# Optimization experiments

Measured on AMD Instinct MI355X. Metric: run time of the kernel, lower is better.

Reference implementation:

```python
import jax, jax.numpy as jnp
import numpy as np

EPS = 1e-5
NEG_INF = float('-inf')

B, L, D = 4, 1024, 1024
H = 16
HD = D // H
I = 3280  # _round_to_multiple(3.2 * 1024, 8)
WIN = 256
STD = 0.01


def rmsnorm(x, w):
    x = jnp.clip(x.astype(jnp.float32), -10000.0, 10000.0)
    rms = jnp.sqrt(jnp.maximum(jnp.mean(x * x, axis=-1, keepdims=True), EPS) + EPS)
    out = x / rms * w
    return jnp.where(jnp.isfinite(out), out, jnp.zeros_like(out))


def setup_inputs() -> dict:
    key = jax.random.key(0)
    ks = jax.random.split(key, 12)
    inp = {
        'x': jax.random.normal(ks[0], (B, L, D), dtype=jnp.float32),
        'wq_w': jax.random.normal(ks[1], (D, D), dtype=jnp.float32) * STD,
        'wq_b': jnp.zeros((D,), jnp.float32),
        'wk_w': jax.random.normal(ks[2], (D, D), dtype=jnp.float32) * STD,
        'wk_b': jnp.zeros((D,), jnp.float32),
        'wv_w': jax.random.normal(ks[3], (D, D), dtype=jnp.float32) * STD,
        'wv_b': jnp.zeros((D,), jnp.float32),
        'wo_w': jax.random.normal(ks[4], (D, D), dtype=jnp.float32) * STD,
        'wo_b': jnp.zeros((D,), jnp.float32),
        'q_norm_w': jnp.ones((HD,), jnp.float32),
        'k_norm_w': jnp.ones((HD,), jnp.float32),
        'seq_norm_w': jnp.ones((D,), jnp.float32),
        'seq_post_norm_w': jnp.ones((D,), jnp.float32),
        'ffn_norm_w': jnp.ones((D,), jnp.float32),
        'ffn_post_norm_w': jnp.ones((D,), jnp.float32),
        'w1_w': jax.random.normal(ks[5], (I, D), dtype=jnp.float32) * STD,
        'w1_b': jnp.zeros((I,), jnp.float32),
        'w2_w': jax.random.normal(ks[6], (D, I), dtype=jnp.float32) * STD,
        'w2_b': jnp.zeros((D,), jnp.float32),
        'w3_w': jax.random.normal(ks[7], (I, D), dtype=jnp.float32) * STD,
        'w3_b': jnp.zeros((I,), jnp.float32),
        'window_size': WIN,
    }
    return inp


def attention(x, wq_w, wq_b, wk_w, wk_b, wv_w, wv_b, wo_w, wo_b, q_norm_w, k_norm_w, window_size):
    b, l, d = x.shape
    x = x.astype(jnp.float32)
    q = (x @ wq_w.T + wq_b).reshape(b, l, H, HD)
    k = (x @ wk_w.T + wk_b).reshape(b, l, H, HD)
    v = (x @ wv_w.T + wv_b).reshape(b, l, H, HD)
    q = rmsnorm(q, q_norm_w)
    k = rmsnorm(k, k_norm_w)
    scale = HD ** -0.5
    scores = jnp.einsum('blhd,bmhd->bhlm', q, k) * scale
    i = jnp.arange(l)[:, None]
    j = jnp.arange(l)[None, :]
    masked = (j > i) | (i - j >= window_size)  # True => forbidden
    scores = scores + jnp.where(masked, NEG_INF, 0.0)
    p = jax.nn.softmax(scores, axis=-1)
    attn = jnp.einsum('bhlm,bmhd->blhd', p, v)
    attn = jnp.where(jnp.isfinite(attn), attn, jnp.zeros_like(attn))
    attn = attn.reshape(b, l, d)
    return attn @ wo_w.T + wo_b


def swiglu(x, w1_w, w1_b, w2_w, w2_b, w3_w, w3_b):
    x = x.astype(jnp.float32)
    z1 = x @ w1_w.T + w1_b
    z3 = x @ w3_w.T + w3_b
    return (jax.nn.silu(z1) * z3) @ w2_w.T + w2_b


def reference(x, wq_w, wq_b, wk_w, wk_b, wv_w, wv_b, wo_w, wo_b,
              q_norm_w, k_norm_w, seq_norm_w, seq_post_norm_w,
              ffn_norm_w, ffn_post_norm_w,
              w1_w, w1_b, w2_w, w2_b, w3_w, w3_b, window_size):
    # seq_norm -> attn -> seq_post_norm -> residual
    a = attention(rmsnorm(x, seq_norm_w), wq_w, wq_b, wk_w, wk_b, wv_w, wv_b,
                  wo_w, wo_b, q_norm_w, k_norm_w, window_size)
    h = x + rmsnorm(a, seq_post_norm_w)
    # ffn_norm -> ffn -> ffn_post_norm -> residual
    f = swiglu(rmsnorm(h, ffn_norm_w), w1_w, w1_b, w2_w, w2_b, w3_w, w3_b)
    return h + rmsnorm(f, ffn_post_norm_w)
```

## Files before the change

### kernel.cpp

```cpp
#include <hip/hip_runtime.h>
#include <cmath>
#include <cstdint>

typedef __bf16 bf16;
typedef bf16 bf16x4 __attribute__((ext_vector_type(4)));
typedef bf16 bf16x8 __attribute__((ext_vector_type(8)));
typedef float f32x4 __attribute__((ext_vector_type(4)));
typedef unsigned int u32;
typedef u32 u32x4 __attribute__((ext_vector_type(4)));

#define EPS 1e-5f

__device__ __forceinline__ float clipf(float v) {
    return fminf(fmaxf(v, -10000.0f), 10000.0f);
}
__device__ __forceinline__ float fin0(float v) { return isfinite(v) ? v : 0.0f; }

__device__ __forceinline__ void async_copy16(void* lds, const void* g) {
    __builtin_amdgcn_global_load_lds((__attribute__((address_space(1))) void*)(void*)g,
                                     (__attribute__((address_space(3))) void*)lds,
                                     16, 0, 0);
}

__global__ __launch_bounds__(256) void prep(const float* __restrict__ wq, const float* __restrict__ wk,
                                            const float* __restrict__ wv, const float* __restrict__ wo,
                                            bf16* __restrict__ Wq, bf16* __restrict__ Wk,
                                            bf16* __restrict__ Wv, bf16* __restrict__ Wo,
                                            const float* __restrict__ w1, const float* __restrict__ w3,
                                            bf16* __restrict__ Wf,
                                            const float* __restrict__ w2, bf16* __restrict__ W2p,
                                            const float* __restrict__ x, const float* __restrict__ snw,
                                            bf16* __restrict__ xn) {
    const int bid = blockIdx.x, t = threadIdx.x;
    if (bid < 4096) {
        int z = bid >> 10, r = bid & 1023;
        const float* in = (z == 0) ? wq : (z == 1) ? wk : (z == 2) ? wv : wo;
        bf16* out = (z == 0) ? Wq : (z == 1) ? Wk : (z == 2) ? Wv : Wo;
        f32x4 v = ((const f32x4*)(in + (size_t)r * 1024))[t];
        bf16x4 o = {(bf16)v[0], (bf16)v[1], (bf16)v[2], (bf16)v[3]};
        ((bf16x4*)(out + (size_t)r * 1024))[t] = o;
    } else if (bid < 10752) {
        int ri = bid - 4096;
        int lc = ((ri >> 5) << 4) + (ri & 15);
        const float* in = ((ri >> 4) & 1) ? w3 : w1;
        bf16x4 o = {(bf16)0.f, (bf16)0.f, (bf16)0.f, (bf16)0.f};
        if (lc < 3280) {
            f32x4 v = ((const f32x4*)(in + (size_t)lc * 1024))[t];
            o[0] = (bf16)v[0]; o[1] = (bf16)v[1]; o[2] = (bf16)v[2]; o[3] = (bf16)v[3];
        }
        ((bf16x4*)(Wf + (size_t)ri * 1024))[t] = o;
    } else if (bid < 11776) {
        int r = bid - 10752;
        for (int c4 = t * 4; c4 < 3328; c4 += 1024) {
            bf16x4 o = {(bf16)0.f, (bf16)0.f, (bf16)0.f, (bf16)0.f};
            if (c4 + 3 < 3280) {
                f32x4 v = *(const f32x4*)(w2 + (size_t)r * 3280 + c4);
                o[0] = (bf16)v[0]; o[1] = (bf16)v[1]; o[2] = (bf16)v[2]; o[3] = (bf16)v[3];
            } else {
                #pragma unroll
                for (int j = 0; j < 4; ++j)
                    if (c4 + j < 3280) o[j] = (bf16)w2[(size_t)r * 3280 + c4 + j];
            }
            *(bf16x4*)(W2p + (size_t)r * 3328 + c4) = o;
        }
    } else {
        __shared__ float sred[4];
        int row = bid - 11776;
        f32x4 xv = ((const f32x4*)(x + (size_t)row * 1024))[t];
        f32x4 cv;
        cv[0] = clipf(xv[0]); cv[1] = clipf(xv[1]); cv[2] = clipf(xv[2]); cv[3] = clipf(xv[3]);
        float ss = cv[0]*cv[0] + cv[1]*cv[1] + cv[2]*cv[2] + cv[3]*cv[3];
        #pragma unroll
        for (int off = 32; off >= 1; off >>= 1) ss += __shfl_xor(ss, off, 64);
        if ((t & 63) == 0) sred[t >> 6] = ss;
        __syncthreads();
        float tot = sred[0] + sred[1] + sred[2] + sred[3];
        float rms = sqrtf(fmaxf(tot * (1.0f / 1024.0f), EPS) + EPS);
        f32x4 wv_ = ((const f32x4*)snw)[t];
        bf16x4 o;
        o[0] = (bf16)fin0(cv[0] / rms * wv_[0]);
        o[1] = (bf16)fin0(cv[1] / rms * wv_[1]);
        o[2] = (bf16)fin0(cv[2] / rms * wv_[2]);
        o[3] = (bf16)fin0(cv[3] / rms * wv_[3]);
        *(bf16x4*)(xn + (size_t)row * 1024 + t * 4) = o;
    }
}

__global__ __launch_bounds__(256) void gemm_qkv(const bf16* __restrict__ A,
                                                const bf16* __restrict__ B0,
                                                const bf16* __restrict__ B1,
                                                const bf16* __restrict__ B2,
                                                const float* __restrict__ g0,
                                                const float* __restrict__ g1,
                                                const float* __restrict__ g2,
                                                const float* __restrict__ qnw,
                                                const float* __restrict__ knw,
                                                bf16* __restrict__ C0,
                                                bf16* __restrict__ C1,
                                                bf16* __restrict__ VT) {
    const int z = blockIdx.z;
    const bf16* B = (z == 0) ? B0 : (z == 1) ? B1 : B2;
    const float* bias = (z == 0) ? g0 : (z == 1) ? g1 : g2;
    const float* hw = (z == 0) ? qnw : knw;

    __shared__ __align__(16) bf16 sA[2][128 * 32];
    __shared__ __align__(16) bf16 sB[2][128 * 32];
    const int tid = threadIdx.x;
    const int w = tid >> 6, lane = tid & 63;
    const int m0 = blockIdx.x * 128;
    const int n0 = blockIdx.y * 128;
    const int mwo = (w >> 1) * 64, nwo = (w & 1) * 64;
    const int r16 = lane & 15, quad = lane >> 4;
    const int kreg = quad * 8;
    const int K = 1024, N = 1024;

    f32x4 zero = {0.f, 0.f, 0.f, 0.f};
    f32x4 acc[4][4];
    #pragma unroll
    for (int i = 0; i < 4; ++i)
        #pragma unroll
        for (int j = 0; j < 4; ++j) acc[i][j] = zero;

    const int c0 = tid, c1 = tid + 256;
    const int am0 = c0 >> 2, ak0 = (c0 & 3) << 3;
    const int am1 = c1 >> 2, ak1 = (c1 & 3) << 3;

    {
        async_copy16(&sA[0][c0 * 8], &A[(size_t)(m0 + am0) * K + ak0]);
        async_copy16(&sA[0][c1 * 8], &A[(size_t)(m0 + am1) * K + ak1]);
        async_copy16(&sB[0][c0 * 8], &B[(size_t)(n0 + am0) * K + ak0]);
        async_copy16(&sB[0][c1 * 8], &B[(size_t)(n0 + am1) * K + ak1]);
    }
    for (int kt = 0; kt < 32; ++kt) {
        __syncthreads();
        const int cur = kt & 1, nxt = cur ^ 1;
        if (kt + 1 < 32) {
            const int kb = (kt + 1) << 5;
            async_copy16(&sA[nxt][c0 * 8], &A[(size_t)(m0 + am0) * K + kb + ak0]);
            async_copy16(&sA[nxt][c1 * 8], &A[(size_t)(m0 + am1) * K + kb + ak1]);
            async_copy16(&sB[nxt][c0 * 8], &B[(size_t)(n0 + am0) * K + kb + ak0]);
            async_copy16(&sB[nxt][c1 * 8], &B[(size_t)(n0 + am1) * K + kb + ak1]);
        }
        bf16x8 af[4], bfr[4];
        #pragma unroll
        for (int i = 0; i < 4; ++i) {
            af[i]  = *(const bf16x8*)&sA[cur][(mwo + i * 16 + r16) * 32 + kreg];
            bfr[i] = *(const bf16x8*)&sB[cur][(nwo + i * 16 + r16) * 32 + kreg];
        }
        #pragma unroll
        for (int mi = 0; mi < 4; ++mi)
            #pragma unroll
            for (int ni = 0; ni < 4; ++ni)
                acc[mi][ni] = __builtin_amdgcn_mfma_f32_16x16x32_bf16(af[mi], bfr[ni], acc[mi][ni], 0, 0, 0);
    }

    float bv[4];
    #pragma unroll
    for (int ni = 0; ni < 4; ++ni) bv[ni] = bias[n0 + nwo + ni * 16 + r16];

    if (z < 2) {
        bf16* C = (z == 0) ? C0 : C1;
        float nwv[4];
        #pragma unroll
        for (int ni = 0; ni < 4; ++ni) nwv[ni] = hw[ni * 16 + r16];
        #pragma unroll
        for (int mi = 0; mi < 4; ++mi) {
            #pragma unroll
            for (int r = 0; r < 4; ++r) {
                float v[4], ss = 0.0f;
                #pragma unroll
                for (int ni = 0; ni < 4; ++ni) {
                    v[ni] = clipf(acc[mi][ni][r] + bv[ni]);
                    ss += v[ni] * v[ni];
                }
                ss += __shfl_xor(ss, 1, 64);
                ss += __shfl_xor(ss, 2, 64);
                ss += __shfl_xor(ss, 4, 64);
                ss += __shfl_xor(ss, 8, 64);
                float rms = sqrtf(fmaxf(ss * (1.0f / 64.0f), EPS) + EPS);
                int row = m0 + mwo + mi * 16 + quad * 4 + r;
                #pragma unroll
                for (int ni = 0; ni < 4; ++ni) {
                    int col = n0 + nwo + ni * 16 + r16;
                    C[(size_t)row * N + col] = (bf16)fin0(v[ni] / rms * nwv[ni]);
                }
            }
        }
    } else {
        const int b_ = m0 >> 10;
        const int tokbase = (m0 & 1023) + mwo;
        #pragma unroll
        for (int ni = 0; ni < 4; ++ni) {
            int col = n0 + nwo + ni * 16 + r16;
            int h_ = col >> 6, hd = col & 63;
            bf16* dst = VT + (((size_t)b_ * 16 + h_) * 64 + hd) * 1024;
            #pragma unroll
            for (int mi = 0; mi < 4; ++mi) {
                bf16x4 pack;
                #pragma unroll
                for (int r = 0; r < 4; ++r) pack[r] = (bf16)(acc[mi][ni][r] + bv[ni]);
                *(bf16x4*)&dst[tokbase + mi * 16 + quad * 4] = pack;
            }
        }
    }
}

__global__ __launch_bounds__(256) void attn_win(const bf16* __restrict__ q,
                                                const bf16* __restrict__ k,
                                                const bf16* __restrict__ vt,
                                                const int* __restrict__ winp,
                                                bf16* __restrict__ o) {
    __shared__ __align__(16) bf16 sQ[64 * 64];
    __shared__ __align__(16) bf16 sK[64 * 64];
    __shared__ __align__(16) bf16 sVt[64 * 80];
    __shared__ __align__(16) bf16 sP[64 * 64];
    const int tid = threadIdx.x, w = tid >> 6, lane = tid & 63;
    const int qt = blockIdx.x, h = blockIdx.y, b = blockIdx.z;
    const int q0 = qt * 64;
    const int win = *winp;
    const float scale = 0.125f;
    const int r16 = lane & 15, quad = lane >> 4;

    {
        int qr0 = tid >> 3, col0 = (tid & 7) * 8;
        async_copy16(&sQ[tid * 8], &q[(((size_t)b * 1024 + q0 + qr0) * 16 + h) * 64 + col0]);
        int c1 = tid + 256;
        int qr1 = c1 >> 3, col1 = (c1 & 7) * 8;
        async_copy16(&sQ[c1 * 8], &q[(((size_t)b * 1024 + q0 + qr1) * 16 + h) * 64 + col1]);
    }
    __syncthreads();
    bf16x8 aq0 = *(const bf16x8*)&sQ[(w * 16 + r16) * 64 + quad * 8];
    bf16x8 aq1 = *(const bf16x8*)&sQ[(w * 16 + r16) * 64 + 32 + quad * 8];

    float Lr[4];
    f32x4 zero = {0.f, 0.f, 0.f, 0.f};
    f32x4 accO[4];
    #pragma unroll
    for (int r = 0; r < 4; ++r) Lr[r] = 0.0f;
    #pragma unroll
    for (int nf = 0; nf < 4; ++nf) accO[nf] = zero;

    int lo = q0 - (win - 1); if (lo < 0) lo = 0;
    const int kt0 = lo >> 6;
    const bf16* vth = vt + ((size_t)b * 16 + h) * 64 * 1024;

    for (int kt = kt0; kt <= qt; ++kt) {
        __syncthreads();
        {
            int col0 = (tid & 7) * 8;
            async_copy16(&sK[tid * 8], &k[(((size_t)b * 1024 + kt * 64 + (tid >> 3)) * 16 + h) * 64 + col0]);
            int c1 = tid + 256;
            int col1 = (c1 & 7) * 8;
            async_copy16(&sK[c1 * 8], &k[(((size_t)b * 1024 + kt * 64 + (c1 >> 3)) * 16 + h) * 64 + col1]);
        }
        #pragma unroll
        for (int c = tid; c < 512; c += 256) {
            int hd = c >> 3, koff = (c & 7) * 8;
            *(u32x4*)&sVt[hd * 80 + koff] = *(const u32x4*)&vth[(size_t)hd * 1024 + kt * 64 + koff];
        }
        __syncthreads();

        f32x4 sf[4];
        #pragma unroll
        for (int nf = 0; nf < 4; ++nf) {
            bf16x8 bk0 = *(const bf16x8*)&sK[(nf * 16 + r16) * 64 + quad * 8];
            bf16x8 bk1 = *(const bf16x8*)&sK[(nf * 16 + r16) * 64 + 32 + quad * 8];
            f32x4 accS = zero;
            accS = __builtin_amdgcn_mfma_f32_16x16x32_bf16(aq0, bk0, accS, 0, 0, 0);
            accS = __builtin_amdgcn_mfma_f32_16x16x32_bf16(aq1, bk1, accS, 0, 0, 0);
            sf[nf] = accS;
        }

        #pragma unroll
        for (int r = 0; r < 4; ++r) {
            int i = q0 + w * 16 + quad * 4 + r;
            float ps = 0.0f;
            #pragma unroll
            for (int nf = 0; nf < 4; ++nf) {
                int j = kt * 64 + nf * 16 + r16;
                bool ok = (j <= i) && (i - j < win);
                float pv = ok ? __expf(sf[nf][r] * scale - 8.0f) : 0.0f;
                ps += pv;
                sP[(w * 16 + quad * 4 + r) * 64 + nf * 16 + r16] = (bf16)pv;
            }
            Lr[r] += ps;
        }
        __syncthreads();

        bf16x8 ap0 = *(const bf16x8*)&sP[(w * 16 + r16) * 64 + quad * 8];
        bf16x8 ap1 = *(const bf16x8*)&sP[(w * 16 + r16) * 64 + 32 + quad * 8];
        #pragma unroll
        for (int nf = 0; nf < 4; ++nf) {
            bf16x8 bv0 = *(const bf16x8*)&sVt[(nf * 16 + r16) * 80 + quad * 8];
            bf16x8 bv1 = *(const bf16x8*)&sVt[(nf * 16 + r16) * 80 + 32 + quad * 8];
            accO[nf] = __builtin_amdgcn_mfma_f32_16x16x32_bf16(ap0, bv0, accO[nf], 0, 0, 0);
            accO[nf] = __builtin_amdgcn_mfma_f32_16x16x32_bf16(ap1, bv1, accO[nf], 0, 0, 0);
        }
    }

    #pragma unroll
    for (int r = 0; r < 4; ++r) {
        float l = Lr[r];
        l += __shfl_xor(l, 1, 64);
        l += __shfl_xor(l, 2, 64);
        l += __shfl_xor(l, 4, 64);
        l += __shfl_xor(l, 8, 64);
        float inv = (l > 0.0f) ? 1.0f / l : 0.0f;
        int row = q0 + w * 16 + quad * 4 + r;
        #pragma unroll
        for (int nf = 0; nf < 4; ++nf) {
            float ov = fin0(accO[nf][r] * inv);
            o[(((size_t)b * 1024 + row) * 16 + h) * 64 + nf * 16 + r16] = (bf16)ov;
        }
    }
}

__global__ __launch_bounds__(512) void gemm_sk2(const bf16* __restrict__ A,
                                                const bf16* __restrict__ B,
                                                float* __restrict__ P,
                                                int K, int Kh) {
    __shared__ __align__(16) bf16 sA[2][256 * 32];
    __shared__ __align__(16) bf16 sB[2][128 * 32];
    const int tid = threadIdx.x;
    const int w = tid >> 6, lane = tid & 63;
    const int m0 = blockIdx.x * 256, n0 = blockIdx.y * 128;
    const int mwo = (w & 3) * 64, nwo = (w >> 2) * 64;
    const int r16 = lane & 15, quad = lane >> 4, kreg = quad * 8;
    const int kbase = blockIdx.z * Kh;
    const int N = 1024;

    const int ar0 = tid >> 2,        ak0 = (tid & 3) << 3;
    const int c1 = tid + 512;
    const int ar1 = c1 >> 2,         ak1 = (c1 & 3) << 3;
    const int br = tid >> 2,         bk = (tid & 3) << 3;

    f32x4 zero = {0.f, 0.f, 0.f, 0.f};
    f32x4 acc[4][4];
    #pragma unroll
    for (int i = 0; i < 4; ++i)
        #pragma unroll
        for (int j = 0; j < 4; ++j) acc[i][j] = zero;

    {
        async_copy16(&sA[0][tid * 8], &A[(size_t)(m0 + ar0) * K + kbase + ak0]);
        async_copy16(&sA[0][c1 * 8],  &A[(size_t)(m0 + ar1) * K + kbase + ak1]);
        async_copy16(&sB[0][tid * 8], &B[(size_t)(n0 + br) * K + kbase + bk]);
    }
    const int kIters = Kh >> 5;
    for (int kt = 0; kt < kIters; ++kt) {
        __syncthreads();
        const int cur = kt & 1, nxt = cur ^ 1;
        if (kt + 1 < kIters) {
            const int kb = kbase + ((kt + 1) << 5);
            async_copy16(&sA[nxt][tid * 8], &A[(size_t)(m0 + ar0) * K + kb + ak0]);
            async_copy16(&sA[nxt][c1 * 8],  &A[(size_t)(m0 + ar1) * K + kb + ak1]);
            async_copy16(&sB[nxt][tid * 8], &B[(size_t)(n0 + br) * K + kb + bk]);
        }
        bf16x8 af[4], bfr[4];
        #pragma unroll
        for (int i = 0; i < 4; ++i) {
            af[i]  = *(const bf16x8*)&sA[cur][(mwo + i * 16 + r16) * 32 + kreg];
            bfr[i] = *(const bf16x8*)&sB[cur][(nwo + i * 16 + r16) * 32 + kreg];
        }
        #pragma unroll
        for (int mi = 0; mi < 4; ++mi)
            #pragma unroll
            for (int ni = 0; ni < 4; ++ni)
                acc[mi][ni] = __builtin_amdgcn_mfma_f32_16x16x32_bf16(af[mi], bfr[ni], acc[mi][ni], 0, 0, 0);
    }

    float* Pz = P + (size_t)blockIdx.z * 4096 * 1024;
    #pragma unroll
    for (int mi = 0; mi < 4; ++mi)
        #pragma unroll
        for (int ni = 0; ni < 4; ++ni) {
            int col = n0 + nwo + ni * 16 + r16;
            #pragma unroll
            for (int r = 0; r < 4; ++r) {
                int row = m0 + mwo + mi * 16 + quad * 4 + r;
                Pz[(size_t)row * N + col] = acc[mi][ni][r];
            }
        }
}

template <bool EMIT>
__global__ __launch_bounds__(512) void resid_norm(const float* __restrict__ xres,
                                                  const float* __restrict__ p0,
                                                  const float* __restrict__ p1,
                                                  const float* __restrict__ bias,
                                                  const float* __restrict__ wpost,
                                                  const float* __restrict__ wnext,
                                                  float* __restrict__ hout,
                                                  bf16* __restrict__ hnout) {
    __shared__ float sred[8];
    const int tid = threadIdx.x;
    const int grp = tid >> 8, t = tid & 255;
    const int w4 = (tid >> 6) & 3;
    for (int it = 0; it < 4; ++it) {
        int row = it * 1024 + blockIdx.x * 2 + grp;
        f32x4 a0 = ((const f32x4*)(p0 + (size_t)row * 1024))[t];
        f32x4 a1 = ((const f32x4*)(p1 + (size_t)row * 1024))[t];
        f32x4 bv = ((const f32x4*)bias)[t];
        f32x4 af;
        af[0] = clipf(a0[0] + a1[0] + bv[0]);
        af[1] = clipf(a0[1] + a1[1] + bv[1]);
        af[2] = clipf(a0[2] + a1[2] + bv[2]);
        af[3] = clipf(a0[3] + a1[3] + bv[3]);
        float ss = af[0]*af[0] + af[1]*af[1] + af[2]*af[2] + af[3]*af[3];
        #pragma unroll
        for (int off = 32; off >= 1; off >>= 1) ss += __shfl_xor(ss, off, 64);
        __syncthreads();
        if ((tid & 63) == 0) sred[grp * 4 + w4] = ss;
        __syncthreads();
        float tot = sred[grp*4+0] + sred[grp*4+1] + sred[grp*4+2] + sred[grp*4+3];
        float rms1 = sqrtf(fmaxf(tot * (1.0f / 1024.0f), EPS) + EPS);
        f32x4 xv = ((const f32x4*)(xres + (size_t)row * 1024))[t];
        f32x4 wp = ((const f32x4*)wpost)[t];
        f32x4 hv;
        hv[0] = xv[0] + fin0(af[0] / rms1 * wp[0]);
        hv[1] = xv[1] + fin0(af[1] / rms1 * wp[1]);
        hv[2] = xv[2] + fin0(af[2] / rms1 * wp[2]);
        hv[3] = xv[3] + fin0(af[3] / rms1 * wp[3]);
        ((f32x4*)(hout + (size_t)row * 1024))[t] = hv;
        if (EMIT) {
            f32x4 cv;
            cv[0] = clipf(hv[0]); cv[1] = clipf(hv[1]); cv[2] = clipf(hv[2]); cv[3] = clipf(hv[3]);
            float ss2 = cv[0]*cv[0] + cv[1]*cv[1] + cv[2]*cv[2] + cv[3]*cv[3];
            #pragma unroll
            for (int off = 32; off >= 1; off >>= 1) ss2 += __shfl_xor(ss2, off, 64);
            __syncthreads();
            if ((tid & 63) == 0) sred[grp * 4 + w4] = ss2;
            __syncthreads();
            float tot2 = sred[grp*4+0] + sred[grp*4+1] + sred[grp*4+2] + sred[grp*4+3];
            float rms2 = sqrtf(fmaxf(tot2 * (1.0f / 1024.0f), EPS) + EPS);
            f32x4 wn = ((const f32x4*)wnext)[t];
            bf16x4 o;
            o[0] = (bf16)fin0(cv[0] / rms2 * wn[0]);
            o[1] = (bf16)fin0(cv[1] / rms2 * wn[1]);
            o[2] = (bf16)fin0(cv[2] / rms2 * wn[2]);
            o[3] = (bf16)fin0(cv[3] / rms2 * wn[3]);
            *(bf16x4*)(hnout + (size_t)row * 1024 + t * 4) = o;
        }
    }
}

template <int MB>
__device__ __forceinline__ void mquad(const bf16x8 (&a)[2][2], const bf16x8 (&breg)[4][2],
                                      f32x4 (&acc)[8][4]) {
    __builtin_amdgcn_s_setprio(1);
    #pragma unroll
    for (int n = 0; n < 4; ++n) {
        acc[MB][n]     = __builtin_amdgcn_mfma_f32_16x16x32_bf16(a[0][0], breg[n][0], acc[MB][n], 0, 0, 0);
        acc[MB][n]     = __builtin_amdgcn_mfma_f32_16x16x32_bf16(a[0][1], breg[n][1], acc[MB][n], 0, 0, 0);
        acc[MB + 1][n] = __builtin_amdgcn_mfma_f32_16x16x32_bf16(a[1][0], breg[n][0], acc[MB + 1][n], 0, 0, 0);
        acc[MB + 1][n] = __builtin_amdgcn_mfma_f32_16x16x32_bf16(a[1][1], breg[n][1], acc[MB + 1][n], 0, 0, 0);
    }
    __builtin_amdgcn_s_setprio(0);
}

__device__ __forceinline__ void aread(const bf16* Ah, int MB, int r16, int koff0, int koff1,
                                      bf16x8 (&a)[2][2]) {
    const bf16* p0 = &Ah[(MB * 16 + r16) * 64];
    const bf16* p1 = &Ah[((MB + 1) * 16 + r16) * 64];
    a[0][0] = *(const bf16x8*)&p0[koff0];
    a[0][1] = *(const bf16x8*)&p0[koff1];
    a[1][0] = *(const bf16x8*)&p1[koff0];
    a[1][1] = *(const bf16x8*)&p1[koff1];
}

__global__ __launch_bounds__(512, 2) void gemm_ffn1_8ph(const bf16* __restrict__ A,
                                                        const bf16* __restrict__ Wf,
                                                        const float* __restrict__ b1,
                                                        const float* __restrict__ b3,
                                                        bf16* __restrict__ G) {
    __shared__ __align__(16) bf16 sA[2][2][128 * 64];
    __shared__ __align__(16) bf16 sB[2][2][128 * 64];
    const int tid = threadIdx.x;
    const int w = tid >> 6, lane = tid & 63;
    const int wr = w >> 2, wc = w & 3;
    const int r16 = lane & 15, quad = lane >> 4;

    const int flat = blockIdx.x;
    const int swb = (flat & 7) * 52 + (flat >> 3);
    const int bm = swb & 15, bn = swb >> 4;
    const int m0 = bm * 256;
    const int n0i = bn * 256;

    const int swz = r16 & 7;
    const int koff0 = ((quad ^ swz) << 3);
    const int koff1 = (((quad + 4) ^ swz) << 3);

    const int sr0 = tid >> 3, sr1 = sr0 + 64;
    const int sk0 = (((tid & 7) ^ (sr0 & 7)) << 3);

    const bf16* aSrc0 = A + (size_t)m0 * 1024;
    const bf16* aSrc1 = A + (size_t)(m0 + 128) * 1024;
    const bf16* bSrc0 = Wf + (size_t)n0i * 1024;
    const bf16* bSrc1 = Wf + (size_t)(n0i + 128) * 1024;

#define STAGE(dst, src, ktile) do {                                                        \
        async_copy16(&(dst)[tid * 8],         (src) + (size_t)sr0 * 1024 + (ktile) * 64 + sk0); \
        async_copy16(&(dst)[(tid + 512) * 8], (src) + (size_t)sr1 * 1024 + (ktile) * 64 + sk0); \
    } while (0)

    f32x4 acc[8][4];
    #pragma unroll
    for (int i = 0; i < 8; ++i)
        #pragma unroll
        for (int j = 0; j < 4; ++j) acc[i][j] = (f32x4){0.f, 0.f, 0.f, 0.f};

    STAGE(sA[0][0], aSrc0, 0); STAGE(sA[0][1], aSrc1, 0);
    STAGE(sB[0][0], bSrc0, 0); STAGE(sB[0][1], bSrc1, 0);
    STAGE(sB[1][0], bSrc0, 1); STAGE(sB[1][1], bSrc1, 1);
    asm volatile("s_waitcnt vmcnt(4)" ::: "memory");
    __builtin_amdgcn_sched_barrier(0);

    for (int t = 0; t < 16; ++t) {
        const int cur = t & 1, nxt = cur ^ 1;
        const bf16* Ah = &sA[cur][wr][0];
        const bf16* Bh = &sB[cur][wc >> 1][0];
        const int rbB = (wc & 1) << 6;

        __builtin_amdgcn_s_barrier();
        if (t + 1 < 16) { STAGE(sA[nxt][0], aSrc0, t + 1); STAGE(sA[nxt][1], aSrc1, t + 1); }

        bf16x8 breg[4][2];
        #pragma unroll
        for (int n = 0; n < 4; ++n) {
            const bf16* p = &Bh[(rbB + n * 16 + r16) * 64];
            breg[n][0] = *(const bf16x8*)&p[koff0];
            breg[n][1] = *(const bf16x8*)&p[koff1];
        }
        bf16x8 a0[2][2], a1[2][2];
        aread(Ah, 0, r16, koff0, koff1, a0);
        aread(Ah, 2, r16, koff0, koff1, a1);
        mquad<0>(a0, breg, acc);

        asm volatile("s_waitcnt lgkmcnt(0)" ::: "memory");
        __builtin_amdgcn_sched_barrier(0);
        __builtin_amdgcn_s_barrier();
        if (t + 2 < 16) { STAGE(sB[cur][0], bSrc0, t + 2); STAGE(sB[cur][1], bSrc1, t + 2); }

        bf16x8 a2[2][2];
        aread(Ah, 4, r16, koff0, koff1, a2);
        mquad<2>(a1, breg, acc);
        bf16x8 a3[2][2];
        aread(Ah, 6, r16, koff0, koff1, a3);
        mquad<4>(a2, breg, acc);
        mquad<6>(a3, breg, acc);

        if (t < 14)       asm volatile("s_waitcnt lgkmcnt(0) vmcnt(4)" ::: "memory");
        else if (t == 14) asm volatile("s_waitcnt lgkmcnt(0) vmcnt(0)" ::: "memory");
        else              asm volatile("s_waitcnt lgkmcnt(0)" ::: "memory");
        __builtin_amdgcn_sched_barrier(0);
    }
#undef STAGE

    #pragma unroll
    for (int m = 0; m < 8; ++m) {
        #pragma unroll
        for (int p = 0; p < 2; ++p) {
            int col = (bn * 8 + wc * 2 + p) * 16 + r16;
            float bb1 = (col < 3280) ? b1[col] : 0.0f;
            float bb3 = (col < 3280) ? b3[col] : 0.0f;
            #pragma unroll
            for (int rr = 0; rr < 4; ++rr) {
                int row = m0 + wr * 128 + m * 16 + quad * 4 + rr;
                float z1 = acc[m][2 * p][rr] + bb1;
                float z3 = acc[m][2 * p + 1][rr] + bb3;
                float s = z1 / (1.0f + __expf(-z1));
                G[(size_t)row * 3328 + col] = (bf16)(s * z3);
            }
        }
    }
}

extern "C" void kernel_launch(void* const* d_in, const int* in_sizes, int n_in,
                              void* d_out, int out_size, void* d_ws, size_t ws_size,
                              hipStream_t stream) {
    const float* x       = (const float*)d_in[0];
    const float* wq_w    = (const float*)d_in[1];
    const float* wq_b    = (const float*)d_in[2];
    const float* wk_w    = (const float*)d_in[3];
    const float* wk_b    = (const float*)d_in[4];
    const float* wv_w    = (const float*)d_in[5];
    const float* wv_b    = (const float*)d_in[6];
    const float* wo_w    = (const float*)d_in[7];
    const float* wo_b    = (const float*)d_in[8];
    const float* q_norm_w= (const float*)d_in[9];
    const float* k_norm_w= (const float*)d_in[10];
    const float* seq_norm_w      = (const float*)d_in[11];
    const float* seq_post_norm_w = (const float*)d_in[12];
    const float* ffn_norm_w      = (const float*)d_in[13];
    const float* ffn_post_norm_w = (const float*)d_in[14];
    const float* w1_w    = (const float*)d_in[15];
    const float* w1_b    = (const float*)d_in[16];
    const float* w2_w    = (const float*)d_in[17];
    const float* w2_b    = (const float*)d_in[18];
    const float* w3_w    = (const float*)d_in[19];
    const float* w3_b    = (const float*)d_in[20];
    const int*   winp    = (const int*)d_in[21];
    float* out = (float*)d_out;

    const size_t SZ_W   = 2097152;
    const size_t SZ_WP  = 6815744;
    const size_t SZ_ACT = 8388608;
    const size_t SZ_H   = 16777216;
    const size_t SZ_P   = 33554432;

    char* p = (char*)d_ws;
    bf16* Wq  = (bf16*)p; p += SZ_W;
    bf16* Wk  = (bf16*)p; p += SZ_W;
    bf16* Wv  = (bf16*)p; p += SZ_W;
    bf16* Wo  = (bf16*)p; p += SZ_W;
    bf16* Wfp = (bf16*)p; p += 2 * SZ_WP;
    bf16* W2p = (bf16*)p; p += SZ_WP;
    float* h  = (float*)p; p += SZ_H;
    bf16* hn  = (bf16*)p; p += SZ_ACT;
    float* part = (float*)p; p += SZ_P;
    float* part1 = part + (size_t)4096 * 1024;
    char* regionA = p;
    bf16* xn    = (bf16*)(regionA);
    bf16* qb    = (bf16*)(regionA + 1 * SZ_ACT);
    bf16* kb    = (bf16*)(regionA + 2 * SZ_ACT);
    bf16* vtb   = (bf16*)(regionA + 3 * SZ_ACT);
    bf16* attnb = (bf16*)(regionA + 4 * SZ_ACT);
    bf16* g     = (bf16*)(regionA);

    prep<<<dim3(15872), dim3(256), 0, stream>>>(wq_w, wk_w, wv_w, wo_w, Wq, Wk, Wv, Wo,
                                                w1_w, w3_w, Wfp, w2_w, W2p,
                                                x, seq_norm_w, xn);

    gemm_qkv<<<dim3(32, 8, 3), dim3(256), 0, stream>>>(xn, Wq, Wk, Wv, wq_b, wk_b, wv_b,
                                                       q_norm_w, k_norm_w, qb, kb, vtb);

    attn_win<<<dim3(16, 16, 4), dim3(256), 0, stream>>>(qb, kb, vtb, winp, attnb);

    gemm_sk2<<<dim3(16, 8, 2), dim3(512), 0, stream>>>(attnb, Wo, part, 1024, 512);

    resid_norm<true><<<dim3(512), dim3(512), 0, stream>>>(x, part, part1, wo_b,
                                                          seq_post_norm_w, ffn_norm_w, h, hn);

    gemm_ffn1_8ph<<<dim3(416), dim3(512), 0, stream>>>(hn, Wfp, w1_b, w3_b, g);

    gemm_sk2<<<dim3(16, 8, 2), dim3(512), 0, stream>>>(g, W2p, part, 3328, 1664);

    resid_norm<false><<<dim3(512), dim3(512), 0, stream>>>(h, part, part1, w2_b,
                                                           ffn_post_norm_w, nullptr, out, nullptr);
}
```

Measured before the change: 387.2 us.

## Software-pipeline the SwiGLU GEMM main loop with finer-grained staged loads

Restructures the W1/W3 GEMM k-loop so the last MFMA quad of each tile is deferred into the next iteration, and global-to-LDS stage copies are split into four smaller chunks interleaved with MFMA quads between extra barriers. It moves the waitcnt to the loop top and changes the initial prefetch order. The intent is to hide LDS read and global load latency better behind compute, at the cost of more s_barriers per iteration and more registers held live across iterations.

```diff
diff --git a/kernel.cpp b/kernel.cpp
--- a/kernel.cpp
+++ b/kernel.cpp
@@ -509,11 +509,12 @@
         #pragma unroll
         for (int j = 0; j < 4; ++j) acc[i][j] = (f32x4){0.f, 0.f, 0.f, 0.f};
 
+    STAGE(sB[0][0], bSrc0, 0); STAGE(sB[0][1], bSrc1, 0);
     STAGE(sA[0][0], aSrc0, 0); STAGE(sA[0][1], aSrc1, 0);
-    STAGE(sB[0][0], bSrc0, 0); STAGE(sB[0][1], bSrc1, 0);
     STAGE(sB[1][0], bSrc0, 1); STAGE(sB[1][1], bSrc1, 1);
-    asm volatile("s_waitcnt vmcnt(4)" ::: "memory");
-    __builtin_amdgcn_sched_barrier(0);
+
+    bf16x8 br[4][2];
+    bf16x8 ah[2][2];
 
     for (int t = 0; t < 16; ++t) {
         const int cur = t & 1, nxt = cur ^ 1;
@@ -521,40 +522,49 @@
         const bf16* Bh = &sB[cur][wc >> 1][0];
         const int rbB = (wc & 1) << 6;
 
+        asm volatile("s_waitcnt lgkmcnt(0)" ::: "memory");
+        if (t < 15) asm volatile("s_waitcnt vmcnt(4)" ::: "memory");
+        else        asm volatile("s_waitcnt vmcnt(0)" ::: "memory");
+        __builtin_amdgcn_sched_barrier(0);
         __builtin_amdgcn_s_barrier();
-        if (t + 1 < 16) { STAGE(sA[nxt][0], aSrc0, t + 1); STAGE(sA[nxt][1], aSrc1, t + 1); }
-
-        bf16x8 breg[4][2];
+        if (t + 1 < 16) STAGE(sA[nxt][0], aSrc0, t + 1);
+        if (t) mquad<6>(ah, br, acc);
+        __builtin_amdgcn_sched_barrier(0);
         #pragma unroll
         for (int n = 0; n < 4; ++n) {
             const bf16* p = &Bh[(rbB + n * 16 + r16) * 64];
-            breg[n][0] = *(const bf16x8*)&p[koff0];
-            breg[n][1] = *(const bf16x8*)&p[koff1];
-        }
-        bf16x8 a0[2][2], a1[2][2];
+            br[n][0] = *(const bf16x8*)&p[koff0];
+            br[n][1] = *(const bf16x8*)&p[koff1];
+        }
+        bf16x8 a0[2][2];
         aread(Ah, 0, r16, koff0, koff1, a0);
-        aread(Ah, 2, r16, koff0, koff1, a1);
-        mquad<0>(a0, breg, acc);
-
-        asm volatile("s_waitcnt lgkmcnt(0)" ::: "memory");
         __builtin_amdgcn_sched_barrier(0);
         __builtin_amdgcn_s_barrier();
-        if (t + 2 < 16) { STAGE(sB[cur][0], bSrc0, t + 2); STAGE(sB[cur][1], bSrc1, t + 2); }
-
+
+        if (t + 1 < 16) STAGE(sA[nxt][1], aSrc1, t + 1);
+        bf16x8 a1[2][2];
+        aread(Ah, 2, r16, koff0, koff1, a1);
+        mquad<0>(a0, br, acc);
+        __builtin_amdgcn_sched_barrier(0);
+        __builtin_amdgcn_s_barrier();
+
+        if (t + 2 < 16) STAGE(sB[cur][0], bSrc0, t + 2);
         bf16x8 a2[2][2];
         aread(Ah, 4, r16, koff0, koff1, a2);
-        mquad<2>(a1, breg, acc);
-        bf16x8 a3[2][2];
-        aread(Ah, 6, r16, koff0, koff1, a3);
-        mquad<4>(a2, breg, acc);
-        mquad<6>(a3, breg, acc);
-
-        if (t < 14)       asm volatile("s_waitcnt lgkmcnt(0) vmcnt(4)" ::: "memory");
-        else if (t == 14) asm volatile("s_waitcnt lgkmcnt(0) vmcnt(0)" ::: "memory");
-        else              asm volatile("s_waitcnt lgkmcnt(0)" ::: "memory");
+        mquad<2>(a1, br, acc);
         __builtin_amdgcn_sched_barrier(0);
+        __builtin_amdgcn_s_barrier();
+
+        if (t + 2 < 16) STAGE(sB[cur][1], bSrc1, t + 2);
+        aread(Ah, 6, r16, koff0, koff1, ah);
+        mquad<4>(a2, br, acc);
+        __builtin_amdgcn_sched_barrier(0);
+        __builtin_amdgcn_s_barrier();
     }
 #undef STAGE
+    asm volatile("s_waitcnt lgkmcnt(0)" ::: "memory");
+    __builtin_amdgcn_sched_barrier(0);
+    mquad<6>(ah, br, acc);
 
     #pragma unroll
     for (int m = 0; m < 8; ++m) {
```

Measured after the change: 374.3 us. 3.3% less time.
